# Kernel tuning notes

Measured on AMD Instinct MI355X. Metric: run time of the kernel, lower is better.

The kernel has to match this reference:

```python
import jax, jax.numpy as jnp
import numpy as np


def setup_inputs() -> dict:
    key = jax.random.key(0)
    k1, k2 = jax.random.split(key)
    codes = jax.random.normal(k1, (32, 512, 64, 64), dtype=jnp.float32)
    # semantic map: integer {0,1} per segment channel at input resolution
    sem = jax.random.randint(k2, (32, 8, 256, 256), 0, 2, dtype=jnp.int32)
    # zero out the last segment channel so the empty-mask fallback branch is exercised
    sem = sem.at[:, -1].set(0)
    return {"codes": codes, "sem": sem}


def _nearest_downsample(sem, hs, ws):
    # matches F.interpolate(mode='nearest'): out[i] = in[floor(i * H_in / H_out)]
    H, W = sem.shape[2], sem.shape[3]
    ih = (jnp.arange(hs) * H) // hs
    iw = (jnp.arange(ws) * W) // ws
    return sem[:, :, ih[:, None], iw[None, :]]  # [bs, s, hs, ws]


def reference(codes, sem):
    bs, cs, hs, ws = codes.shape
    s_size = sem.shape[1]
    segmap = _nearest_downsample(sem, hs, ws)          # [bs, s, hs, ws] int
    mask = (segmap != 0).astype(codes.dtype)           # bool-as-float mask
    area = mask.sum(axis=(-2, -1))                     # [bs, s]
    # masked per-channel sums over spatial dims (fused segment reduce)
    sums = jnp.einsum('bchw,bshw->bsc', codes, mask)   # [bs, s, c]
    seg_mean = sums / jnp.maximum(area, 1.0)[..., None]
    # fallback for empty masks: global per-channel spatial mean (calc_mean_std mean)
    glob_mean = codes.mean(axis=(2, 3))                # [bs, c]
    codes_vector = jnp.where(area[..., None] > 0, seg_mean, glob_mean[:, None, :])
    return codes_vector.reshape(bs, -1)[:, :, None, None]  # [bs, s*c, 1, 1]
```

## Files before the change

### kernel.cpp

```cpp
#include <hip/hip_runtime.h>
#include <hip/hip_bf16.h>


#define BS    32
#define CS    512
#define SEG   8
#define HS    64
#define WS    64
#define HW    (HS*WS)
#define SEMH  256
#define SEMW  256
#define NCHUNK 16
#define CPB   2

__global__ __launch_bounds__(256) void mask_area_kernel(
    const int* __restrict__ sem,
    unsigned char* __restrict__ mask8,
    int* __restrict__ partial)
{
    const int blk   = blockIdx.x;
    const int b     = blk >> 4;
    const int chunk = blk & (NCHUNK - 1);
    const int t     = threadIdx.x;

    const int hw = chunk * 256 + t;
    const int h  = hw >> 6;
    const int w  = hw & 63;
    const int* p = sem + (size_t)b * SEG * SEMH * SEMW + (h * 4) * SEMW + (w * 4);

    unsigned int m = 0;
#pragma unroll
    for (int s = 0; s < SEG; ++s)
        if (p[s * (SEMH * SEMW)] != 0) m |= (1u << s);
    mask8[b * HW + hw] = (unsigned char)m;

    __shared__ int redc[4][SEG];
    const int lane = t & 63, wv = t >> 6;
#pragma unroll
    for (int s = 0; s < SEG; ++s) {
        unsigned long long bal = __ballot((m >> s) & 1u);
        if (lane == 0) redc[wv][s] = __popcll(bal);
    }
    __syncthreads();
    if (t < SEG)
        partial[(b * NCHUNK + chunk) * SEG + t] =
            redc[0][t] + redc[1][t] + redc[2][t] + redc[3][t];
}

__global__ __launch_bounds__(256) void seg_mean_kernel(
    const float* __restrict__ codes,
    const unsigned char* __restrict__ mask8,
    const int* __restrict__ partial,
    float* __restrict__ out)
{
    const int blk = blockIdx.x;
    const int b   = blk >> 8;
    const int c0  = (blk & 255) * CPB;
    const int t   = threadIdx.x;

    const float* src = codes + ((size_t)b * CS + c0) * HW;
    const unsigned char* mb = mask8 + b * HW;

    float acc[CPB][SEG + 1];
#pragma unroll
    for (int cc = 0; cc < CPB; ++cc)
#pragma unroll
        for (int s = 0; s <= SEG; ++s) acc[cc][s] = 0.0f;

#pragma unroll
    for (int i = 0; i < 4; ++i) {
        const int hw = i * 1024 + t * 4;
        const unsigned int m4 = *reinterpret_cast<const unsigned int*>(mb + hw);
#pragma unroll
        for (int cc = 0; cc < CPB; ++cc) {
            const float4 v = *reinterpret_cast<const float4*>(src + cc * HW + hw);
            const float vals[4] = { v.x, v.y, v.z, v.w };
#pragma unroll
            for (int p = 0; p < 4; ++p) {
                const float val = vals[p];
                const unsigned int m = m4 >> (8 * p);
                acc[cc][SEG] += val;
#pragma unroll
                for (int s = 0; s < SEG; ++s)
                    acc[cc][s] += (m & (1u << s)) ? val : 0.0f;
            }
        }
    }

#pragma unroll
    for (int off = 32; off; off >>= 1)
#pragma unroll
        for (int cc = 0; cc < CPB; ++cc)
#pragma unroll
            for (int s = 0; s <= SEG; ++s)
                acc[cc][s] += __shfl_down(acc[cc][s], off);

    __shared__ float red[4][CPB][SEG + 1];
    const int lane = t & 63, wv = t >> 6;
    if (lane == 0) {
#pragma unroll
        for (int cc = 0; cc < CPB; ++cc)
#pragma unroll
            for (int s = 0; s <= SEG; ++s) red[wv][cc][s] = acc[cc][s];
    }
    __syncthreads();

    if (t < SEG) {
        int ai = 0;
#pragma unroll
        for (int k = 0; k < NCHUNK; ++k)
            ai += partial[(b * NCHUNK + k) * SEG + t];
        const float a = (float)ai;
#pragma unroll
        for (int cc = 0; cc < CPB; ++cc) {
            const float seg  = red[0][cc][t]   + red[1][cc][t]   + red[2][cc][t]   + red[3][cc][t];
            const float glob = red[0][cc][SEG] + red[1][cc][SEG] + red[2][cc][SEG] + red[3][cc][SEG];
            out[b * (SEG * CS) + t * CS + (c0 + cc)] =
                (a > 0.0f) ? (seg / a) : (glob * (1.0f / (float)HW));
        }
    }
}

extern "C" void kernel_launch(void* const* d_in, const int* in_sizes, int n_in,
                              void* d_out, int out_size, void* d_ws, size_t ws_size,
                              hipStream_t stream) {
    const float* codes = (const float*)d_in[0];
    const int*   sem   = (const int*)d_in[1];
    float*       out   = (float*)d_out;

    unsigned char* mask8   = (unsigned char*)d_ws;
    int*           partial = (int*)((char*)d_ws + BS * HW);

    mask_area_kernel<<<BS * NCHUNK, 256, 0, stream>>>(sem, mask8, partial);
    seg_mean_kernel<<<BS * CS / CPB, 256, 0, stream>>>(codes, mask8, partial, out);
}
```

Before: 61.41 us.

## Use single-wave blocks with mul24 bit-spread mask weights and FMA accumulation

Shrinks the seg-mean blocks from 256 to 64 threads, so one wavefront walks the whole 4096-element plane and the shared-memory reduction and __syncthreads go away. Mask bits are expanded into 0/1 float weights with a multiply-and-mask trick and accumulated with fmaf instead of per-bit selects. Butterfly xor shuffles are used so every lane ends with the totals. The cost is fewer threads per block and 16 serial loop iterations per thread, which raises per-thread latency and relies on many resident blocks to keep memory busy.

```diff
diff --git a/kernel.cpp b/kernel.cpp
--- a/kernel.cpp
+++ b/kernel.cpp
@@ -47,7 +47,7 @@
             redc[0][t] + redc[1][t] + redc[2][t] + redc[3][t];
 }
 
-__global__ __launch_bounds__(256) void seg_mean_kernel(
+__global__ __launch_bounds__(64) void seg_mean_kernel(
     const float* __restrict__ codes,
     const unsigned char* __restrict__ mask8,
     const int* __restrict__ partial,
@@ -56,67 +56,79 @@
     const int blk = blockIdx.x;
     const int b   = blk >> 8;
     const int c0  = (blk & 255) * CPB;
-    const int t   = threadIdx.x;
+    const int l   = threadIdx.x;
 
     const float* src = codes + ((size_t)b * CS + c0) * HW;
     const unsigned char* mb = mask8 + b * HW;
 
-    float acc[CPB][SEG + 1];
+    float acc[CPB][SEG];
+    float gl[CPB];
 #pragma unroll
-    for (int cc = 0; cc < CPB; ++cc)
+    for (int cc = 0; cc < CPB; ++cc) {
+        gl[cc] = 0.0f;
 #pragma unroll
-        for (int s = 0; s <= SEG; ++s) acc[cc][s] = 0.0f;
+        for (int s = 0; s < SEG; ++s) acc[cc][s] = 0.0f;
+    }
 
 #pragma unroll
-    for (int i = 0; i < 4; ++i) {
-        const int hw = i * 1024 + t * 4;
+    for (int i = 0; i < 16; ++i) {
+        const int hw = i * 256 + l * 4;
         const unsigned int m4 = *reinterpret_cast<const unsigned int*>(mb + hw);
+        const float4 v0 = *reinterpret_cast<const float4*>(src + hw);
+        const float4 v1 = *reinterpret_cast<const float4*>(src + HW + hw);
+        const float va[CPB][4] = { { v0.x, v0.y, v0.z, v0.w },
+                                   { v1.x, v1.y, v1.z, v1.w } };
 #pragma unroll
-        for (int cc = 0; cc < CPB; ++cc) {
-            const float4 v = *reinterpret_cast<const float4*>(src + cc * HW + hw);
-            const float vals[4] = { v.x, v.y, v.z, v.w };
+        for (int p = 0; p < 4; ++p) {
+            const unsigned int lo = (m4 >> (8 * p)) & 0xFu;
+            const unsigned int hi = (m4 >> (8 * p + 4)) & 0xFu;
+            const unsigned int slo = ((unsigned int)__mul24((int)lo, 0x00204081)) & 0x01010101u;
+            const unsigned int shi = ((unsigned int)__mul24((int)hi, 0x00204081)) & 0x01010101u;
+            float w[SEG];
+            w[0] = (float)( slo        & 0xffu);
+            w[1] = (float)((slo >> 8)  & 0xffu);
+            w[2] = (float)((slo >> 16) & 0xffu);
+            w[3] = (float)( slo >> 24        );
+            w[4] = (float)( shi        & 0xffu);
+            w[5] = (float)((shi >> 8)  & 0xffu);
+            w[6] = (float)((shi >> 16) & 0xffu);
+            w[7] = (float)( shi >> 24        );
 #pragma unroll
-            for (int p = 0; p < 4; ++p) {
-                const float val = vals[p];
-                const unsigned int m = m4 >> (8 * p);
-                acc[cc][SEG] += val;
+            for (int cc = 0; cc < CPB; ++cc) {
+                const float val = va[cc][p];
+                gl[cc] += val;
 #pragma unroll
                 for (int s = 0; s < SEG; ++s)
-                    acc[cc][s] += (m & (1u << s)) ? val : 0.0f;
+                    acc[cc][s] = fmaf(val, w[s], acc[cc][s]);
             }
         }
     }
 
 #pragma unroll
-    for (int off = 32; off; off >>= 1)
+    for (int off = 32; off; off >>= 1) {
 #pragma unroll
-        for (int cc = 0; cc < CPB; ++cc)
+        for (int cc = 0; cc < CPB; ++cc) {
+            gl[cc] += __shfl_xor(gl[cc], off);
 #pragma unroll
-            for (int s = 0; s <= SEG; ++s)
-                acc[cc][s] += __shfl_down(acc[cc][s], off);
+            for (int s = 0; s < SEG; ++s)
+                acc[cc][s] += __shfl_xor(acc[cc][s], off);
+        }
+    }
 
-    __shared__ float red[4][CPB][SEG + 1];
-    const int lane = t & 63, wv = t >> 6;
-    if (lane == 0) {
-#pragma unroll
-        for (int cc = 0; cc < CPB; ++cc)
-#pragma unroll
-            for (int s = 0; s <= SEG; ++s) red[wv][cc][s] = acc[cc][s];
-    }
-    __syncthreads();
-
-    if (t < SEG) {
+    if (l < SEG) {
         int ai = 0;
 #pragma unroll
         for (int k = 0; k < NCHUNK; ++k)
-            ai += partial[(b * NCHUNK + k) * SEG + t];
+            ai += partial[(b * NCHUNK + k) * SEG + l];
         const float a = (float)ai;
 #pragma unroll
         for (int cc = 0; cc < CPB; ++cc) {
-            const float seg  = red[0][cc][t]   + red[1][cc][t]   + red[2][cc][t]   + red[3][cc][t];
-            const float glob = red[0][cc][SEG] + red[1][cc][SEG] + red[2][cc][SEG] + red[3][cc][SEG];
-            out[b * (SEG * CS) + t * CS + (c0 + cc)] =
-                (a > 0.0f) ? (seg / a) : (glob * (1.0f / (float)HW));
+            float seg = 0.0f;
+#pragma unroll
+            for (int s = 0; s < SEG; ++s)
+                seg = (l == s) ? acc[cc][s] : seg;
+            out[b * (SEG * CS) + l * CS + (c0 + cc)] =
+                (a > 0.0f) ? (seg / a) : (gl[cc] * (1.0f / (float)HW));
         }
     }
 }
@@ -132,5 +144,5 @@
     int*           partial = (int*)((char*)d_ws + BS * HW);
 
     mask_area_kernel<<<BS * NCHUNK, 256, 0, stream>>>(sem, mask8, partial);
-    seg_mean_kernel<<<BS * CS / CPB, 256, 0, stream>>>(codes, mask8, partial, out);
+    seg_mean_kernel<<<BS * CS / CPB, 64, 0, stream>>>(codes, mask8, partial, out);
 }
```

After: 57.39 us. 1.07x faster.
